# Kernel optimization log

Measured on AMD Instinct MI355X. Metric: run time of the kernel, lower is better.

The kernel has to match this reference:

```python
import jax, jax.numpy as jnp
import numpy as np

N = 100000   # nodes
E = 1600000  # edges
G = 1024     # graphs
V = 51       # attr_dims[0]+1 embedding rows (padding_idx=0)
EMB = 32
H = 2        # heads
D = 64       # hidden_dim (per-head out channels)
DC = H * D   # 128 = dim_conv
NEG_GAT = 0.2   # PyG GATConv default negative_slope
NEG_ACT = 0.05  # module's leaky_relu slope
LN_EPS = 1e-5


def setup_inputs() -> dict:
    key = jax.random.key(0)
    ks = jax.random.split(key, 20)
    def nrm(k, shape, scale=0.1):
        return jax.random.normal(k, shape, dtype=jnp.float32) * scale
    x = jax.random.randint(ks[0], (N, 1), 0, V)
    edge_index = jax.random.randint(ks[1], (2, E), 0, N)
    batch_idx = jnp.sort(jax.random.randint(ks[2], (N,), 0, G))
    return {
        'x': x, 'edge_index': edge_index, 'batch_idx': batch_idx,
        'emb': nrm(ks[3], (V, EMB)).at[0].set(0.0),  # padding_idx=0
        'ln_g': jnp.ones((EMB,), jnp.float32), 'ln_b': jnp.zeros((EMB,), jnp.float32),
        'W1': nrm(ks[4], (EMB, DC)), 'a_src1': nrm(ks[5], (H, D)), 'a_dst1': nrm(ks[6], (H, D)), 'b1': nrm(ks[7], (DC,)),
        'W2': nrm(ks[8], (DC, DC)), 'a_src2': nrm(ks[9], (H, D)), 'a_dst2': nrm(ks[10], (H, D)), 'b2': nrm(ks[11], (DC,)),
        'gw1': nrm(ks[12], (DC, D)), 'gb1': nrm(ks[13], (D,)),
        'gw2': nrm(ks[14], (D, 1)), 'gb2': nrm(ks[15], (1,)),
    }


def _gat_conv(xf, src, dst, W, a_src, a_dst, b):
    # xf: [N, in]; returns [N, H*D]. PyG GATConv, eval mode (attn dropout off).
    xw = (xf @ W).reshape(N, H, D)                           # [N,H,D]
    al_s = jnp.einsum('nhd,hd->nh', xw, a_src)
    al_d = jnp.einsum('nhd,hd->nh', xw, a_dst)
    e = jax.nn.leaky_relu(al_s[src] + al_d[dst], NEG_GAT)    # [E',H]
    m = jax.ops.segment_max(e, dst, num_segments=N)
    ex = jnp.exp(e - m[dst])
    s = jax.ops.segment_sum(ex, dst, num_segments=N)
    alpha = ex / s[dst]                                      # segment softmax over incoming edges
    msg = xw[src] * alpha[:, :, None]                        # [E',H,D]
    out = jax.ops.segment_sum(msg, dst, num_segments=N)      # [N,H,D]
    return out.reshape(N, DC) + b


def reference(x, edge_index, batch_idx, emb, ln_g, ln_b,
              W1, a_src1, a_dst1, b1, W2, a_src2, a_dst2, b2,
              gw1, gb1, gw2, gb2):
    # embedding + LayerNorm (dropout off in eval)
    xe = emb[x[:, 0]]                                        # [N,32]
    mu = jnp.mean(xe, axis=-1, keepdims=True)
    var = jnp.var(xe, axis=-1, keepdims=True)
    xe = (xe - mu) * jax.lax.rsqrt(var + LN_EPS) * ln_g + ln_b
    # add self loops (GATConv add_self_loops=True)
    ar = jnp.arange(N, dtype=edge_index.dtype)
    src = jnp.concatenate([edge_index[0], ar])
    dst = jnp.concatenate([edge_index[1], ar])
    h = jax.nn.leaky_relu(_gat_conv(xe, src, dst, W1, a_src1, a_dst1, b1), NEG_ACT)
    h = _gat_conv(h, src, dst, W2, a_src2, a_dst2, b2)       # [N,128]
    # attentional aggregation over graphs
    gate = jax.nn.leaky_relu(h @ gw1 + gb1, NEG_ACT) @ gw2 + gb2   # [N,1]
    gm = jax.ops.segment_max(gate, batch_idx, num_segments=G)
    ge = jnp.exp(gate - gm[batch_idx])
    gs = jax.ops.segment_sum(ge, batch_idx, num_segments=G)
    w = ge / gs[batch_idx]
    z = jax.ops.segment_sum(w * h, batch_idx, num_segments=G)      # [G,128]
    return h, z
```

## Files before the change

kernel.cpp:

```cpp
#include <hip/hip_runtime.h>
#include <hip/hip_bf16.h>
#include <stdint.h>

typedef unsigned short u16;
typedef unsigned int   u32;
typedef __attribute__((ext_vector_type(8))) short bf16x8;
typedef __attribute__((ext_vector_type(4))) float f32x4;

#define NEG_GAT 0.2f
#define NEG_ACT 0.05f
#define LN_EPS  1e-5f
#define NPARAM  15

__device__ __forceinline__ float bf2f(u32 bits16){
  union { u32 u; float f; } v; v.u = bits16 << 16; return v.f;
}
__device__ __forceinline__ u16 f2bf(float f){
  union { float f; u32 u; } v; v.f = f;
  u32 u = v.u;
  u32 r = (u + 0x7fffu + ((u >> 16) & 1u)) >> 16;
  return (u16)r;
}
__device__ __forceinline__ float lrelu(float x, float s){ return x > 0.f ? x : s * x; }

__device__ __forceinline__ int geti(const int* __restrict__ p, int i, int enc){
  return p[enc ? (2 * i) : i];
}


struct CvtParams {
  const void* src[NPARAM];
  float*      dst[NPARAM];
  int         n[NPARAM];
};

__global__ void k_detect(const u32* __restrict__ ln_g_raw, const int* __restrict__ ei_raw,
                         int* __restrict__ fflag, int* __restrict__ iflag,
                         int* __restrict__ errflag)
{
  if (threadIdx.x == 0){
    *fflag = (ln_g_raw[0] == 0x3F800000u) ? 0 : 1;
    int zeros = 0;
    for (int j = 0; j < 64; j++) if (ei_raw[2 * j + 1] == 0) zeros++;
    *iflag = (zeros >= 60) ? 1 : 0;
    *errflag = 0;
  }
}

__global__ void k_convert(CvtParams P, const int* __restrict__ flag)
{
  const int pi  = blockIdx.y;
  const int idx = blockIdx.x * 256 + threadIdx.x;
  if (idx >= P.n[pi]) return;
  if (*flag == 0) P.dst[pi][idx] = ((const float*)P.src[pi])[idx];
  else            P.dst[pi][idx] = bf2f(((const u16*)P.src[pi])[idx]);
}


__global__ void k_check_sorted(const int* __restrict__ batch, const int* __restrict__ iflag,
                               int n, int* __restrict__ errflag)
{
  int i = blockIdx.x * 256 + threadIdx.x;
  if (i < n - 1){
    if (geti(batch, i, *iflag) > geti(batch, i + 1, *iflag)) atomicOr(errflag, 8);
  }
}

__global__ void k_check_x(const int* __restrict__ x, const int* __restrict__ iflag,
                          int n, int V, int* __restrict__ errflag)
{
  int i = blockIdx.x * 256 + threadIdx.x;
  if (i < n){
    int v = geti(x, i, *iflag);
    if ((unsigned)v >= (unsigned)V) atomicOr(errflag, 16);
  }
}

__global__ void k_check_edges(const int* __restrict__ ei, const int* __restrict__ iflag,
                              int E, int n, int* __restrict__ errflag)
{
  int e = blockIdx.x * 256 + threadIdx.x;
  if (e < E){
    int enc = *iflag;
    int s = geti(ei, e, enc);
    int d = geti(ei, E + e, enc);
    if ((unsigned)s >= (unsigned)n || (unsigned)d >= (unsigned)n) atomicOr(errflag, 32);
  }
}


__global__ void k_hist(const int* __restrict__ ei, const int* __restrict__ iflag,
                       int* __restrict__ counts, int E, int n)
{
  int e = blockIdx.x * 256 + threadIdx.x;
  if (e < E){
    int d = geti(ei, E + e, *iflag);
    d = min(max(d, 0), n - 1);
    atomicAdd(&counts[d], 1);
  }
}

__global__ void k_scanA(const int* __restrict__ counts, int* __restrict__ rowptr,
                        int* __restrict__ bsums, int n)
{
  __shared__ int sd[1024];
  int tid = threadIdx.x;
  int gid = blockIdx.x * 1024 + tid;
  int v = (gid < n) ? counts[gid] : 0;
  sd[tid] = v;
  __syncthreads();
  for (int off = 1; off < 1024; off <<= 1){
    int t = 0;
    if (tid >= off) t = sd[tid - off];
    __syncthreads();
    if (tid >= off) sd[tid] += t;
    __syncthreads();
  }
  if (gid < n) rowptr[gid] = sd[tid] - v;
  if (tid == 1023) bsums[blockIdx.x] = sd[1023];
}

__global__ void k_scanB(const int* __restrict__ bsums, int* __restrict__ boffs, int nb)
{
  __shared__ int sd[128];
  int tid = threadIdx.x;
  int v = (tid < nb) ? bsums[tid] : 0;
  sd[tid] = v;
  __syncthreads();
  for (int off = 1; off < 128; off <<= 1){
    int t = 0;
    if (tid >= off) t = sd[tid - off];
    __syncthreads();
    if (tid >= off) sd[tid] += t;
    __syncthreads();
  }
  if (tid < nb) boffs[tid] = sd[tid] - v;
}

__global__ void k_scanC(int* __restrict__ rowptr, const int* __restrict__ boffs,
                        int* __restrict__ cursor, int n, int Etot)
{
  int gid = blockIdx.x * 1024 + threadIdx.x;
  if (gid < n){
    int v = rowptr[gid] + boffs[blockIdx.x];
    rowptr[gid] = v;
    cursor[gid] = v;
  }
  if (gid == 0) rowptr[n] = Etot;
}

__global__ void k_scatter(const int* __restrict__ ei, const int* __restrict__ iflag,
                          int* __restrict__ cursor, int* __restrict__ csr, int E, int n)
{
  int e = blockIdx.x * 256 + threadIdx.x;
  if (e < E){
    int enc = *iflag;
    int s = geti(ei, e, enc);
    int d = geti(ei, E + e, enc);
    d = min(max(d, 0), n - 1);
    int pos = atomicAdd(&cursor[d], 1);
    csr[pos] = s;
  }
}

__global__ void k_check_rows(const int* __restrict__ rowptr, const int* __restrict__ cursor,
                             int n, int* __restrict__ errflag)
{
  int i = blockIdx.x * 256 + threadIdx.x;
  if (i < n){
    if (cursor[i] != rowptr[i + 1]) atomicOr(errflag, 1);
    if (i == 0 && rowptr[0] != 0)   atomicOr(errflag, 4);
  }
}

__global__ void k_check_csr(const int* __restrict__ csr, int E, int n, int* __restrict__ errflag)
{
  int e = blockIdx.x * 256 + threadIdx.x;
  if (e < E && (unsigned)csr[e] >= (unsigned)n) atomicOr(errflag, 2);
}


#define BSH   9
#define BSZ   512
#define BMSK  511
#define MAXB  2048
#define BINB  8192
#define BTH   512

__global__ void k_bhist(const int* __restrict__ ei, const int* __restrict__ iflag,
                        int* __restrict__ bcnt, int E, int N, int nbuck)
{
  __shared__ int h[MAXB];
  const int t = threadIdx.x;
  for (int i = t; i < nbuck; i += 256) h[i] = 0;
  __syncthreads();
  const int enc = *iflag;
  for (int e = blockIdx.x * 256 + t; e < E; e += gridDim.x * 256){
    int d = geti(ei, E + e, enc);
    d = min(max(d, 0), N - 1);
    atomicAdd(&h[d >> BSH], 1);
  }
  __syncthreads();
  for (int i = t; i < nbuck; i += 256){
    int c = h[i];
    if (c) atomicAdd(&bcnt[i], c);
  }
}

__global__ void k_bscan(const int* __restrict__ bcnt, int* __restrict__ boff,
                        int* __restrict__ gcur, int* __restrict__ rowptr,
                        int nbuck, int N, int E)
{
  __shared__ int sd[MAXB];
  const int lane = threadIdx.x;
  for (int i = lane; i < nbuck; i += 64) sd[i] = bcnt[i];
  __syncthreads();
  const int L = (nbuck + 63) >> 6;
  const int b0 = lane * L;
  int sum = 0;
  for (int j = 0; j < L; j++){ int idx = b0 + j; if (idx < nbuck) sum += sd[idx]; }
  int excl = sum;
  for (int off = 1; off < 64; off <<= 1){
    int x = __shfl_up(excl, off);
    if (lane >= off) excl += x;
  }
  excl -= sum;
  int run = excl;
  for (int j = 0; j < L; j++){
    int idx = b0 + j;
    if (idx < nbuck){ boff[idx] = run; gcur[idx] = run; run += sd[idx]; }
  }
  if (lane == 0){ boff[nbuck] = E; rowptr[N] = E; }
}

__global__ __launch_bounds__(BTH) void k_bbin(
    const int* __restrict__ ei, const int* __restrict__ iflag,
    int* __restrict__ gcur, u32* __restrict__ binned,
    int E, int N, int nbuck)
{
  __shared__ u32 stage[BINB];
  __shared__ u16 sbk[BINB];
  __shared__ int hist[MAXB];
  __shared__ int base[MAXB];
  __shared__ int gpos[MAXB];
  const int t   = threadIdx.x;
  const int e0  = blockIdx.x * BINB;
  const int cnt = min(BINB, E - e0);
  const int enc = *iflag;

  for (int i = t; i < nbuck; i += BTH) hist[i] = 0;
  __syncthreads();

  u32 pv[16]; int bk[16]; int rk[16];
  #pragma unroll
  for (int k = 0; k < 16; k++){
    bk[k] = -1;
    int lo = k * BTH + t;
    if (lo < cnt){
      int e = e0 + lo;
      int s = geti(ei, e, enc);
      int d = geti(ei, E + e, enc);
      s = min(max(s, 0), N - 1);
      d = min(max(d, 0), N - 1);
      int b = d >> BSH;
      pv[k] = ((u32)s << BSH) | (u32)(d & BMSK);
      bk[k] = b;
      rk[k] = atomicAdd(&hist[b], 1);
    }
  }
  __syncthreads();

  if (t < 64){
    const int L = (nbuck + 63) >> 6;
    const int b0 = t * L;
    int sum = 0;
    for (int j = 0; j < L; j++){ int idx = b0 + j; if (idx < nbuck) sum += hist[idx]; }
    int excl = sum;
    for (int off = 1; off < 64; off <<= 1){
      int x = __shfl_up(excl, off);
      if (t >= off) excl += x;
    }
    excl -= sum;
    int run = excl;
    for (int j = 0; j < L; j++){
      int idx = b0 + j;
      if (idx < nbuck){ base[idx] = run; run += hist[idx]; }
    }
  }
  __syncthreads();

  for (int i = t; i < nbuck; i += BTH){
    int c = hist[i];
    gpos[i] = c ? atomicAdd(&gcur[i], c) : 0;
  }
  __syncthreads();

  #pragma unroll
  for (int k = 0; k < 16; k++){
    if (bk[k] >= 0){
      int slot = base[bk[k]] + rk[k];
      stage[slot] = pv[k];
      sbk[slot]   = (u16)bk[k];
    }
  }
  __syncthreads();

  for (int j = t; j < cnt; j += BTH){
    int b = sbk[j];
    binned[gpos[b] + (j - base[b])] = stage[j];
  }
}

__global__ __launch_bounds__(256) void k_bcsr(
    const u32* __restrict__ binned, const int* __restrict__ boff,
    int* __restrict__ rowptr, int* __restrict__ csr, int N, int nbuck)
{
  __shared__ int cnt[BSZ];
  __shared__ int rp[BSZ];
  __shared__ int cur[BSZ];
  const int b = blockIdx.x;
  const int t = threadIdx.x;
  const int lo = boff[b], hi = boff[b + 1];

  for (int i = t; i < BSZ; i += 256){ cnt[i] = 0; cur[i] = 0; }
  __syncthreads();

  for (int j = lo + t; j < hi; j += 256)
    atomicAdd(&cnt[binned[j] & BMSK], 1);
  __syncthreads();

  if (t < 64){
    const int b0 = t * 8;
    int sum = 0;
    #pragma unroll
    for (int j = 0; j < 8; j++) sum += cnt[b0 + j];
    int excl = sum;
    for (int off = 1; off < 64; off <<= 1){
      int x = __shfl_up(excl, off);
      if (t >= off) excl += x;
    }
    excl -= sum;
    int run = excl;
    #pragma unroll
    for (int j = 0; j < 8; j++){ rp[b0 + j] = run; run += cnt[b0 + j]; }
  }
  __syncthreads();

  const int node0 = b << BSH;
  for (int i = t; i < BSZ; i += 256){
    int node = node0 + i;
    if (node < N) rowptr[node] = lo + rp[i];
  }

  for (int j = lo + t; j < hi; j += 256){
    u32 pvv = binned[j];
    int dl  = pvv & BMSK;
    int pos = lo + rp[dl] + atomicAdd(&cur[dl], 1);
    csr[pos] = (int)(pvv >> BSH);
  }
}


__global__ void k_stamp_if(const int* __restrict__ errflag, float* __restrict__ out, int nel)
{
  int f = *errflag;
  if (f == 0) return;
  float s = 500.0f + 100.0f * (float)f;
  int i = blockIdx.x * 256 + threadIdx.x;
  if (i < nel) out[i] = s;
}

__global__ void k_stamp(float* __restrict__ out, int nel, float val)
{
  int i = blockIdx.x * 256 + threadIdx.x;
  if (i < nel) out[i] = val;
}


__global__ void k_prep(const float* __restrict__ emb,
                       const float* __restrict__ ln_g, const float* __restrict__ ln_b,
                       const float* __restrict__ W1, const float* __restrict__ a_src,
                       const float* __restrict__ a_dst,
                       u16* __restrict__ xwv, float* __restrict__ alsv, float* __restrict__ aldv)
{
  __shared__ float se[32];
  __shared__ float stats[2];
  __shared__ float sxw[128];
  const int v = blockIdx.x, t = threadIdx.x;
  if (t < 32) se[t] = emb[v * 32 + t];
  __syncthreads();
  if (t == 0){
    float s1 = 0.f, s2 = 0.f;
    for (int k = 0; k < 32; k++){ s1 += se[k]; s2 += se[k] * se[k]; }
    float mu = s1 * (1.f / 32.f);
    float var = s2 * (1.f / 32.f) - mu * mu;
    stats[0] = mu; stats[1] = rsqrtf(var + LN_EPS);
  }
  __syncthreads();
  const float mu = stats[0], rs = stats[1];
  float o = 0.f;
  for (int k = 0; k < 32; k++){
    float xe = (se[k] - mu) * rs * ln_g[k] + ln_b[k];
    o += xe * W1[k * 128 + t];
  }
  sxw[t] = o;
  xwv[v * 128 + t] = f2bf(o);
  __syncthreads();
  if (t < 2){
    float ps = 0.f, pd = 0.f;
    for (int d = 0; d < 64; d++){
      float vv = sxw[t * 64 + d];
      ps += vv * a_src[t * 64 + d];
      pd += vv * a_dst[t * 64 + d];
    }
    alsv[2 * v + t] = ps;
    aldv[2 * v + t] = pd;
  }
}

__global__ void k_lookup(const int* __restrict__ x, const int* __restrict__ iflag,
                         const u16* __restrict__ xwv, const float* __restrict__ alsv,
                         const float* __restrict__ aldv, int N, int V,
                         u16* __restrict__ xw, float* __restrict__ al_s, float* __restrict__ al_d)
{
  const int enc = *iflag;
  const int tid = threadIdx.x;
  const int c = tid & 15;
  for (int base = blockIdx.x * 16; base < N; base += gridDim.x * 16){
    int i = base + (tid >> 4);
    if (i < N){
      int v = geti(x, i, enc);
      v = min(max(v, 0), V - 1);
      uint4 row = *(const uint4*)(xwv + v * 128 + c * 8);
      *(uint4*)(xw + (size_t)i * 128 + c * 8) = row;
      if (c == 0){ float2 a = *(const float2*)(alsv + 2 * v); *(float2*)(al_s + 2 * i) = a; }
      if (c == 1){ float2 a = *(const float2*)(aldv + 2 * v); *(float2*)(al_d + 2 * i) = a; }
    }
  }
}


__global__ __launch_bounds__(64, 8) void k_gatw(
    const int* __restrict__ rowptr, const int* __restrict__ csr,
    const float* __restrict__ al_s, const float* __restrict__ al_d,
    const u16* __restrict__ xw, const float* __restrict__ bias,
    int apply_act, float* __restrict__ out)
{
  const int i    = blockIdx.x;
  const int lane = threadIdx.x;
  const int sub  = lane >> 4;
  const int c16  = lane & 15;
  const int r0 = rowptr[i], deg = rowptr[i + 1] - r0, total = deg + 1;
  const float ad0 = al_d[2 * i], ad1 = al_d[2 * i + 1];

  float m0 = -3.0e38f, m1 = -3.0e38f;
  for (int k = lane; k < total; k += 64){
    int s = (k < deg) ? csr[r0 + k] : i;
    float a0 = lrelu(al_s[2 * s]     + ad0, NEG_GAT);
    float a1 = lrelu(al_s[2 * s + 1] + ad1, NEG_GAT);
    m0 = fmaxf(m0, a0); m1 = fmaxf(m1, a1);
  }
  #pragma unroll
  for (int off = 32; off; off >>= 1){
    m0 = fmaxf(m0, __shfl_xor(m0, off));
    m1 = fmaxf(m1, __shfl_xor(m1, off));
  }

  float sum0 = 0.f, sum1 = 0.f;
  float acc[8];
  #pragma unroll
  for (int r = 0; r < 8; r++) acc[r] = 0.f;

  for (int base = 0; base < total; base += 64){
    int k = base + lane;
    int s = i; float ex0 = 0.f, ex1 = 0.f;
    if (k < total){
      s = (k < deg) ? csr[r0 + k] : i;
      ex0 = __expf(lrelu(al_s[2 * s]     + ad0, NEG_GAT) - m0);
      ex1 = __expf(lrelu(al_s[2 * s + 1] + ad1, NEG_GAT) - m1);
    }
    sum0 += ex0; sum1 += ex1;

    int cnt  = min(64, total - base);
    int qmax = (cnt + 3) & ~3;
    for (int q = 0; q < qmax; q += 4){
      int   j  = q + sub;
      int   sj = __shfl(s, j);
      float e0 = __shfl(ex0, j);
      float e1 = __shfl(ex1, j);
      float ej = (c16 < 8) ? e0 : e1;
      uint4 w = *(const uint4*)(xw + (size_t)sj * 128 + c16 * 8);
      acc[0] += ej * bf2f(w.x & 0xffffu); acc[1] += ej * bf2f(w.x >> 16);
      acc[2] += ej * bf2f(w.y & 0xffffu); acc[3] += ej * bf2f(w.y >> 16);
      acc[4] += ej * bf2f(w.z & 0xffffu); acc[5] += ej * bf2f(w.z >> 16);
      acc[6] += ej * bf2f(w.w & 0xffffu); acc[7] += ej * bf2f(w.w >> 16);
    }
  }
  #pragma unroll
  for (int off = 32; off; off >>= 1){
    sum0 += __shfl_xor(sum0, off);
    sum1 += __shfl_xor(sum1, off);
  }
  #pragma unroll
  for (int r = 0; r < 8; r++){
    acc[r] += __shfl_xor(acc[r], 16);
    acc[r] += __shfl_xor(acc[r], 32);
  }

  if (sub == 0){
    float inv = 1.f / ((c16 < 8) ? sum0 : sum1);
    const float4* bp = (const float4*)(bias + c16 * 8);
    float4 b0 = bp[0], b1 = bp[1];
    float4 o0, o1;
    o0.x = acc[0] * inv + b0.x; o0.y = acc[1] * inv + b0.y;
    o0.z = acc[2] * inv + b0.z; o0.w = acc[3] * inv + b0.w;
    o1.x = acc[4] * inv + b1.x; o1.y = acc[5] * inv + b1.y;
    o1.z = acc[6] * inv + b1.z; o1.w = acc[7] * inv + b1.w;
    if (apply_act){
      o0.x = lrelu(o0.x, NEG_ACT); o0.y = lrelu(o0.y, NEG_ACT);
      o0.z = lrelu(o0.z, NEG_ACT); o0.w = lrelu(o0.w, NEG_ACT);
      o1.x = lrelu(o1.x, NEG_ACT); o1.y = lrelu(o1.y, NEG_ACT);
      o1.z = lrelu(o1.z, NEG_ACT); o1.w = lrelu(o1.w, NEG_ACT);
    }
    float* op = out + (size_t)i * 128 + c16 * 8;
    *(float4*)op       = o0;
    *(float4*)(op + 4) = o1;
  }
}


__global__ void k_packW(const float* __restrict__ W, int ncols, int ntiles,
                        u16* __restrict__ pb)
{
  const int ktile = blockIdx.x / ntiles;
  const int ntile = blockIdx.x % ntiles;
  const int lane  = threadIdx.x;
  const int n  = ntile * 16 + (lane & 15);
  const int k0 = ktile * 32 + (lane >> 4) * 8;
  u16* dst = pb + ((size_t)blockIdx.x * 64 + lane) * 8;
  #pragma unroll
  for (int j = 0; j < 8; j++)
    dst[j] = f2bf(W[(k0 + j) * ncols + n]);
}


__global__ __launch_bounds__(256, 2) void k_node2m(
    const float* __restrict__ h1, const u16* __restrict__ pb2,
    const float* __restrict__ a_src, const float* __restrict__ a_dst,
    int N, u16* __restrict__ xw, float* __restrict__ al_s, float* __restrict__ al_d)
{
  const int wave = threadIdx.x >> 6;
  const int lane = threadIdx.x & 63;
  const int rowbase = blockIdx.x * 64 + wave * 16;
  const int m    = lane & 15;
  const int quad = lane >> 4;

  int arow = rowbase + m; if (arow >= N) arow = N - 1;
  const float* aptr = h1 + (size_t)arow * 128 + quad * 8;

  f32x4 acc[8];
  #pragma unroll
  for (int nt = 0; nt < 8; nt++) acc[nt] = (f32x4){0.f, 0.f, 0.f, 0.f};

  #pragma unroll
  for (int kt = 0; kt < 4; kt++){
    float4 a0 = *(const float4*)(aptr + kt * 32);
    float4 a1 = *(const float4*)(aptr + kt * 32 + 4);
    bf16x8 af;
    af[0] = (short)f2bf(a0.x); af[1] = (short)f2bf(a0.y);
    af[2] = (short)f2bf(a0.z); af[3] = (short)f2bf(a0.w);
    af[4] = (short)f2bf(a1.x); af[5] = (short)f2bf(a1.y);
    af[6] = (short)f2bf(a1.z); af[7] = (short)f2bf(a1.w);
    const u16* bbase = pb2 + (((size_t)kt * 8) * 64 + lane) * 8;
    #pragma unroll
    for (int nt = 0; nt < 8; nt++){
      bf16x8 bf = *(const bf16x8*)(bbase + (size_t)nt * 64 * 8);
      acc[nt] = __builtin_amdgcn_mfma_f32_16x16x32_bf16(af, bf, acc[nt], 0, 0, 0);
    }
  }

  float asv[8], adv[8];
  #pragma unroll
  for (int nt = 0; nt < 8; nt++){
    asv[nt] = a_src[nt * 16 + m];
    adv[nt] = a_dst[nt * 16 + m];
  }
  #pragma unroll
  for (int r = 0; r < 4; r++){
    int row = rowbase + quad * 4 + r;
    bool ok = row < N;
    float s0 = 0.f, s1 = 0.f, d0 = 0.f, d1 = 0.f;
    #pragma unroll
    for (int nt = 0; nt < 8; nt++){
      float v = acc[nt][r];
      if (ok) xw[(size_t)row * 128 + nt * 16 + m] = f2bf(v);
      if (nt < 4){ s0 += v * asv[nt]; d0 += v * adv[nt]; }
      else       { s1 += v * asv[nt]; d1 += v * adv[nt]; }
    }
    #pragma unroll
    for (int off = 1; off < 16; off <<= 1){
      s0 += __shfl_xor(s0, off); s1 += __shfl_xor(s1, off);
      d0 += __shfl_xor(d0, off); d1 += __shfl_xor(d1, off);
    }
    if (ok && m == 0){
      al_s[2 * row] = s0; al_s[2 * row + 1] = s1;
      al_d[2 * row] = d0; al_d[2 * row + 1] = d1;
    }
  }
}


__global__ __launch_bounds__(256, 2) void k_gatem(
    const float* __restrict__ h, const u16* __restrict__ pbg,
    const float* __restrict__ gb1, const float* __restrict__ gw2,
    const float* __restrict__ gb2, int N, float* __restrict__ gate)
{
  const int wave = threadIdx.x >> 6;
  const int lane = threadIdx.x & 63;
  const int rowbase = blockIdx.x * 64 + wave * 16;
  const int m    = lane & 15;
  const int quad = lane >> 4;

  int arow = rowbase + m; if (arow >= N) arow = N - 1;
  const float* aptr = h + (size_t)arow * 128 + quad * 8;

  f32x4 acc[4];
  #pragma unroll
  for (int nt = 0; nt < 4; nt++) acc[nt] = (f32x4){0.f, 0.f, 0.f, 0.f};

  #pragma unroll
  for (int kt = 0; kt < 4; kt++){
    float4 a0 = *(const float4*)(aptr + kt * 32);
    float4 a1 = *(const float4*)(aptr + kt * 32 + 4);
    bf16x8 af;
    af[0] = (short)f2bf(a0.x); af[1] = (short)f2bf(a0.y);
    af[2] = (short)f2bf(a0.z); af[3] = (short)f2bf(a0.w);
    af[4] = (short)f2bf(a1.x); af[5] = (short)f2bf(a1.y);
    af[6] = (short)f2bf(a1.z); af[7] = (short)f2bf(a1.w);
    const u16* bbase = pbg + (((size_t)kt * 4) * 64 + lane) * 8;
    #pragma unroll
    for (int nt = 0; nt < 4; nt++){
      bf16x8 bf = *(const bf16x8*)(bbase + (size_t)nt * 64 * 8);
      acc[nt] = __builtin_amdgcn_mfma_f32_16x16x32_bf16(af, bf, acc[nt], 0, 0, 0);
    }
  }

  float gbv[4], g2v[4];
  #pragma unroll
  for (int nt = 0; nt < 4; nt++){
    gbv[nt] = gb1[nt * 16 + m];
    g2v[nt] = gw2[nt * 16 + m];
  }
  const float g2b = gb2[0];
  #pragma unroll
  for (int r = 0; r < 4; r++){
    int row = rowbase + quad * 4 + r;
    float q = 0.f;
    #pragma unroll
    for (int nt = 0; nt < 4; nt++)
      q += lrelu(acc[nt][r] + gbv[nt], NEG_ACT) * g2v[nt];
    #pragma unroll
    for (int off = 1; off < 16; off <<= 1) q += __shfl_xor(q, off);
    if (row < N && m == 0) gate[row] = q + g2b;
  }
}


__global__ void k_graphsw(const int* __restrict__ batch, const int* __restrict__ iflag,
                          const float* __restrict__ gate,
                          const float* __restrict__ h, float* __restrict__ zout, int N)
{
  __shared__ int   range[2];
  __shared__ float red[4];
  const int g = blockIdx.x, t = threadIdx.x;
  const int wave = t >> 6;
  if (t == 0){
    const int enc = *iflag;
    int lo = 0, hi = N;
    while (lo < hi){ int mid = (lo + hi) >> 1; if (geti(batch, mid, enc) < g) lo = mid + 1; else hi = mid; }
    range[0] = lo;
    hi = N;
    while (lo < hi){ int mid = (lo + hi) >> 1; if (geti(batch, mid, enc) < g + 1) lo = mid + 1; else hi = mid; }
    range[1] = lo;
  }
  __syncthreads();
  const int st = range[0], en = range[1];

  float m = -3.0e38f;
  for (int k = st + t; k < en; k += 128) m = fmaxf(m, gate[k]);
  #pragma unroll
  for (int off = 32; off; off >>= 1) m = fmaxf(m, __shfl_xor(m, off));
  if ((t & 63) == 0) red[wave] = m;
  __syncthreads();
  m = fmaxf(red[0], red[1]);

  float s = 0.f;
  for (int k = st + t; k < en; k += 128) s += __expf(gate[k] - m);
  #pragma unroll
  for (int off = 32; off; off >>= 1) s += __shfl_xor(s, off);
  if ((t & 63) == 0) red[2 + wave] = s;
  __syncthreads();
  s = red[2] + red[3];

  float z = 0.f;
  const float inv = 1.f / s;
  for (int k = st; k < en; k++){
    float wk = __expf(gate[k] - m) * inv;
    z += wk * h[(size_t)k * 128 + t];
  }
  zout[(size_t)g * 128 + t] = z;
}


extern "C" void kernel_launch(void* const* d_in, const int* in_sizes, int n_in,
                              void* d_out, int out_size, void* d_ws, size_t ws_size,
                              hipStream_t stream)
{
  const int* x      = (const int*)d_in[0];
  const int* ei     = (const int*)d_in[1];
  const int* batch  = (const int*)d_in[2];

  const int N = in_sizes[0];
  const int E = in_sizes[1] / 2;
  const int V = in_sizes[3] / 32;
  const int G = out_size / 128 - N;

  char* p = (char*)d_ws;
  auto alloc = [&](size_t bytes) -> char* {
    char* r = p; p += (bytes + 255) & ~(size_t)255; return r;
  };
  int*   multi  = (int*)  alloc((size_t)N * 4);
  int*   rowptr = (int*)  alloc((size_t)(N + 1) * 4);
  int*   csr    = (int*)  alloc((size_t)E * 4);
  int*   bsums  = (int*)  alloc(4096);
  int*   boffs  = (int*)  alloc(4096);
  int*   flags  = (int*)  alloc(256);
  int*   fflag  = flags;
  int*   iflag  = flags + 1;
  int*   errflg = flags + 2;
  float* al_s   = (float*)alloc((size_t)N * 2 * 4);
  float* al_d   = (float*)alloc((size_t)N * 2 * 4);
  u16*   xw     = (u16*)  alloc((size_t)N * 128 * 2);
  u16*   xwv    = (u16*)  alloc((size_t)V * 128 * 2);
  float* alsv   = (float*)alloc((size_t)V * 2 * 4);
  float* aldv   = (float*)alloc((size_t)V * 2 * 4);
  u16*   pb2    = (u16*)  alloc((size_t)128 * 128 * 2);
  u16*   pbg    = (u16*)  alloc((size_t)128 * 64 * 2);

  const int nbuck = (N + BSZ - 1) >> BSH;
  int*   bcnt   = (int*)  alloc((size_t)(MAXB) * 4);
  int*   boff   = (int*)  alloc((size_t)(MAXB + 1) * 4);
  int*   gcur   = (int*)  alloc((size_t)(MAXB) * 4);
  u32*   binned = (u32*)  alloc((size_t)E * 4);

  CvtParams cp;
  float* fpar[NPARAM];
  int maxn = 0;
  for (int pi = 0; pi < NPARAM; pi++){
    int n = in_sizes[3 + pi];
    fpar[pi] = (float*)alloc((size_t)n * 4);
    cp.src[pi] = d_in[3 + pi];
    cp.dst[pi] = fpar[pi];
    cp.n[pi]   = n;
    if (n > maxn) maxn = n;
  }
  const size_t needed = (size_t)(p - (char*)d_ws);

  const float* emb    = fpar[0];
  const float* ln_g   = fpar[1];
  const float* ln_b   = fpar[2];
  const float* W1     = fpar[3];
  const float* a_src1 = fpar[4];
  const float* a_dst1 = fpar[5];
  const float* b1     = fpar[6];
  const float* W2     = fpar[7];
  const float* a_src2 = fpar[8];
  const float* a_dst2 = fpar[9];
  const float* b2     = fpar[10];
  const float* gw1    = fpar[11];
  const float* gb1    = fpar[12];
  const float* gw2    = fpar[13];
  const float* gb2    = fpar[14];
  (void)n_in;

  int ob = (out_size + 255) / 256;
  if (ws_size < needed){
    k_stamp<<<ob, 256, 0, stream>>>((float*)d_out, out_size, 9999.0f);
    return;
  }

  int*   counts = multi;
  int*   cursor = multi;
  float* gate   = (float*)multi;
  float* hbuf   = (float*)d_out;
  float* zbuf   = (float*)d_out + (size_t)N * 128;

  k_detect<<<1, 64, 0, stream>>>((const u32*)d_in[4], ei, fflag, iflag, errflg);
  dim3 cgrid((maxn + 255) / 256, NPARAM);
  k_convert<<<cgrid, 256, 0, stream>>>(cp, fflag);

  int eb = (E + 255) / 256;
  int nb = (N + 1023) / 1024;
  int nb256 = (N + 255) / 256;

  k_check_sorted<<<nb256, 256, 0, stream>>>(batch, iflag, N, errflg);
  k_check_x<<<nb256, 256, 0, stream>>>(x, iflag, N, V, errflg);
  k_check_edges<<<eb, 256, 0, stream>>>(ei, iflag, E, N, errflg);

  if (nbuck <= MAXB){
    hipMemsetAsync(bcnt, 0, (size_t)nbuck * 4, stream);
    k_bhist<<<256, 256, 0, stream>>>(ei, iflag, bcnt, E, N, nbuck);
    k_bscan<<<1, 64, 0, stream>>>(bcnt, boff, gcur, rowptr, nbuck, N, E);
    k_bbin<<<(E + BINB - 1) / BINB, BTH, 0, stream>>>(ei, iflag, gcur, binned, E, N, nbuck);
    k_bcsr<<<nbuck, 256, 0, stream>>>(binned, boff, rowptr, csr, N, nbuck);
  } else {
    hipMemsetAsync(counts, 0, (size_t)N * 4, stream);
    hipMemsetAsync(csr, 0xFF, (size_t)E * 4, stream);
    k_hist<<<eb, 256, 0, stream>>>(ei, iflag, counts, E, N);
    k_scanA<<<nb, 1024, 0, stream>>>(counts, rowptr, bsums, N);
    k_scanB<<<1, 128, 0, stream>>>(bsums, boffs, nb);
    k_scanC<<<nb, 1024, 0, stream>>>(rowptr, boffs, cursor, N, E);
    k_scatter<<<eb, 256, 0, stream>>>(ei, iflag, cursor, csr, E, N);
    k_check_rows<<<nb256, 256, 0, stream>>>(rowptr, cursor, N, errflg);
    k_check_csr<<<eb, 256, 0, stream>>>(csr, E, N, errflg);
  }

  k_packW<<<32, 64, 0, stream>>>(W2, 128, 8, pb2);
  k_packW<<<16, 64, 0, stream>>>(gw1, 64, 4, pbg);

  k_prep<<<V, 128, 0, stream>>>(emb, ln_g, ln_b, W1, a_src1, a_dst1, xwv, alsv, aldv);
  k_lookup<<<1024, 256, 0, stream>>>(x, iflag, xwv, alsv, aldv, N, V, xw, al_s, al_d);

  k_gatw<<<N, 64, 0, stream>>>(rowptr, csr, al_s, al_d, xw, b1, 1, hbuf);

  const int gblk = (N + 63) / 64;
  k_node2m<<<gblk, 256, 0, stream>>>(hbuf, pb2, a_src2, a_dst2, N, xw, al_s, al_d);

  k_gatw<<<N, 64, 0, stream>>>(rowptr, csr, al_s, al_d, xw, b2, 0, hbuf);

  k_gatem<<<gblk, 256, 0, stream>>>(hbuf, pbg, gb1, gw2, gb2, N, gate);
  k_graphsw<<<G, 128, 0, stream>>>(batch, iflag, gate, hbuf, zbuf, N);

  k_stamp_if<<<ob, 256, 0, stream>>>(errflg, (float*)d_out, out_size);
}
```

Measured before the change: 421.4 us.

## Fuse embedding lookup into first GAT layer and single-pass softmax for small degrees

```diff
diff --git a/kernel.cpp b/kernel.cpp
--- a/kernel.cpp
+++ b/kernel.cpp
@@ -21,7 +21,7 @@
   u32 r = (u + 0x7fffu + ((u >> 16) & 1u)) >> 16;
   return (u16)r;
 }
-__device__ __forceinline__ float lrelu(float x, float s){ return x > 0.f ? x : s * x; }
+__device__ __forceinline__ float lrelu(float x, float s){ return fmaxf(x, s * x); }
 
 __device__ __forceinline__ int geti(const int* __restrict__ p, int i, int enc){
   return p[enc ? (2 * i) : i];
@@ -418,29 +418,131 @@
   }
 }
 
-__global__ void k_lookup(const int* __restrict__ x, const int* __restrict__ iflag,
-                         const u16* __restrict__ xwv, const float* __restrict__ alsv,
-                         const float* __restrict__ aldv, int N, int V,
-                         u16* __restrict__ xw, float* __restrict__ al_s, float* __restrict__ al_d)
-{
-  const int enc = *iflag;
-  const int tid = threadIdx.x;
-  const int c = tid & 15;
-  for (int base = blockIdx.x * 16; base < N; base += gridDim.x * 16){
-    int i = base + (tid >> 4);
-    if (i < N){
-      int v = geti(x, i, enc);
-      v = min(max(v, 0), V - 1);
-      uint4 row = *(const uint4*)(xwv + v * 128 + c * 8);
-      *(uint4*)(xw + (size_t)i * 128 + c * 8) = row;
-      if (c == 0){ float2 a = *(const float2*)(alsv + 2 * v); *(float2*)(al_s + 2 * i) = a; }
-      if (c == 1){ float2 a = *(const float2*)(aldv + 2 * v); *(float2*)(al_d + 2 * i) = a; }
-    }
-  }
-}
-
-
-__global__ __launch_bounds__(64, 8) void k_gatw(
+
+__global__ __launch_bounds__(64, 8) void k_gatw1(
+    const int* __restrict__ rowptr, const int* __restrict__ csr,
+    const int* __restrict__ x, const int* __restrict__ iflag,
+    const float* __restrict__ alsv, const float* __restrict__ aldv,
+    const u16* __restrict__ xwv, const float* __restrict__ bias,
+    int V, float* __restrict__ out)
+{
+  const int i    = blockIdx.x;
+  const int lane = threadIdx.x;
+  const int sub  = lane >> 4;
+  const int c16  = lane & 15;
+  const int enc  = *iflag;
+  const int r0 = rowptr[i], deg = rowptr[i + 1] - r0, total = deg + 1;
+  int vi = geti(x, i, enc); vi = min(max(vi, 0), V - 1);
+  const float ad0 = aldv[2 * vi], ad1 = aldv[2 * vi + 1];
+
+  float sum0 = 0.f, sum1 = 0.f;
+  float acc[8];
+  #pragma unroll
+  for (int r = 0; r < 8; r++) acc[r] = 0.f;
+
+  if (total <= 64){
+    int vs = vi;
+    float a0 = -3.0e38f, a1 = -3.0e38f;
+    if (lane < total){
+      int s = (lane < deg) ? csr[r0 + lane] : i;
+      int v = geti(x, s, enc);
+      vs = min(max(v, 0), V - 1);
+      float2 as = *(const float2*)(alsv + 2 * vs);
+      a0 = lrelu(as.x + ad0, NEG_GAT);
+      a1 = lrelu(as.y + ad1, NEG_GAT);
+    }
+    float m0 = a0, m1 = a1;
+    #pragma unroll
+    for (int off = 32; off; off >>= 1){
+      m0 = fmaxf(m0, __shfl_xor(m0, off));
+      m1 = fmaxf(m1, __shfl_xor(m1, off));
+    }
+    float ex0 = 0.f, ex1 = 0.f;
+    if (lane < total){ ex0 = __expf(a0 - m0); ex1 = __expf(a1 - m1); }
+    sum0 = ex0; sum1 = ex1;
+    int qmax = (total + 3) & ~3;
+    for (int q = 0; q < qmax; q += 4){
+      int   j  = q + sub;
+      int   vj = __shfl(vs, j);
+      float e0 = __shfl(ex0, j);
+      float e1 = __shfl(ex1, j);
+      float ej = (c16 < 8) ? e0 : e1;
+      uint4 w = *(const uint4*)(xwv + (size_t)vj * 128 + c16 * 8);
+      acc[0] += ej * bf2f(w.x & 0xffffu); acc[1] += ej * bf2f(w.x >> 16);
+      acc[2] += ej * bf2f(w.y & 0xffffu); acc[3] += ej * bf2f(w.y >> 16);
+      acc[4] += ej * bf2f(w.z & 0xffffu); acc[5] += ej * bf2f(w.z >> 16);
+      acc[6] += ej * bf2f(w.w & 0xffffu); acc[7] += ej * bf2f(w.w >> 16);
+    }
+  } else {
+    float m0 = -3.0e38f, m1 = -3.0e38f;
+    for (int k = lane; k < total; k += 64){
+      int s = (k < deg) ? csr[r0 + k] : i;
+      int v = geti(x, s, enc); v = min(max(v, 0), V - 1);
+      float2 as = *(const float2*)(alsv + 2 * v);
+      m0 = fmaxf(m0, lrelu(as.x + ad0, NEG_GAT));
+      m1 = fmaxf(m1, lrelu(as.y + ad1, NEG_GAT));
+    }
+    #pragma unroll
+    for (int off = 32; off; off >>= 1){
+      m0 = fmaxf(m0, __shfl_xor(m0, off));
+      m1 = fmaxf(m1, __shfl_xor(m1, off));
+    }
+    for (int base = 0; base < total; base += 64){
+      int k = base + lane;
+      int vs = vi; float ex0 = 0.f, ex1 = 0.f;
+      if (k < total){
+        int s = (k < deg) ? csr[r0 + k] : i;
+        int v = geti(x, s, enc); vs = min(max(v, 0), V - 1);
+        float2 as = *(const float2*)(alsv + 2 * vs);
+        ex0 = __expf(lrelu(as.x + ad0, NEG_GAT) - m0);
+        ex1 = __expf(lrelu(as.y + ad1, NEG_GAT) - m1);
+      }
+      sum0 += ex0; sum1 += ex1;
+      int cnt = min(64, total - base);
+      int qmax = (cnt + 3) & ~3;
+      for (int q = 0; q < qmax; q += 4){
+        int   j  = q + sub;
+        int   vj = __shfl(vs, j);
+        float e0 = __shfl(ex0, j);
+        float e1 = __shfl(ex1, j);
+        float ej = (c16 < 8) ? e0 : e1;
+        uint4 w = *(const uint4*)(xwv + (size_t)vj * 128 + c16 * 8);
+        acc[0] += ej * bf2f(w.x & 0xffffu); acc[1] += ej * bf2f(w.x >> 16);
+        acc[2] += ej * bf2f(w.y & 0xffffu); acc[3] += ej * bf2f(w.y >> 16);
+        acc[4] += ej * bf2f(w.z & 0xffffu); acc[5] += ej * bf2f(w.z >> 16);
+        acc[6] += ej * bf2f(w.w & 0xffffu); acc[7] += ej * bf2f(w.w >> 16);
+      }
+    }
+  }
+
+  #pragma unroll
+  for (int off = 32; off; off >>= 1){
+    sum0 += __shfl_xor(sum0, off);
+    sum1 += __shfl_xor(sum1, off);
+  }
+  #pragma unroll
+  for (int r = 0; r < 8; r++){
+    acc[r] += __shfl_xor(acc[r], 16);
+    acc[r] += __shfl_xor(acc[r], 32);
+  }
+
+  if (sub == 0){
+    float inv = 1.f / ((c16 < 8) ? sum0 : sum1);
+    const float4* bp = (const float4*)(bias + c16 * 8);
+    float4 b0 = bp[0], b1 = bp[1];
+    float4 o0, o1;
+    o0.x = lrelu(acc[0] * inv + b0.x, NEG_ACT); o0.y = lrelu(acc[1] * inv + b0.y, NEG_ACT);
+    o0.z = lrelu(acc[2] * inv + b0.z, NEG_ACT); o0.w = lrelu(acc[3] * inv + b0.w, NEG_ACT);
+    o1.x = lrelu(acc[4] * inv + b1.x, NEG_ACT); o1.y = lrelu(acc[5] * inv + b1.y, NEG_ACT);
+    o1.z = lrelu(acc[6] * inv + b1.z, NEG_ACT); o1.w = lrelu(acc[7] * inv + b1.w, NEG_ACT);
+    float* op = out + (size_t)i * 128 + c16 * 8;
+    *(float4*)op       = o0;
+    *(float4*)(op + 4) = o1;
+  }
+}
+
+
+__global__ __launch_bounds__(64, 8) void k_gatw2(
     const int* __restrict__ rowptr, const int* __restrict__ csr,
     const float* __restrict__ al_s, const float* __restrict__ al_d,
     const u16* __restrict__ xw, const float* __restrict__ bias,
@@ -451,38 +553,32 @@
   const int sub  = lane >> 4;
   const int c16  = lane & 15;
   const int r0 = rowptr[i], deg = rowptr[i + 1] - r0, total = deg + 1;
-  const float ad0 = al_d[2 * i], ad1 = al_d[2 * i + 1];
-
-  float m0 = -3.0e38f, m1 = -3.0e38f;
-  for (int k = lane; k < total; k += 64){
-    int s = (k < deg) ? csr[r0 + k] : i;
-    float a0 = lrelu(al_s[2 * s]     + ad0, NEG_GAT);
-    float a1 = lrelu(al_s[2 * s + 1] + ad1, NEG_GAT);
-    m0 = fmaxf(m0, a0); m1 = fmaxf(m1, a1);
-  }
-  #pragma unroll
-  for (int off = 32; off; off >>= 1){
-    m0 = fmaxf(m0, __shfl_xor(m0, off));
-    m1 = fmaxf(m1, __shfl_xor(m1, off));
-  }
+  const float2 ad = *(const float2*)(al_d + 2 * i);
 
   float sum0 = 0.f, sum1 = 0.f;
   float acc[8];
   #pragma unroll
   for (int r = 0; r < 8; r++) acc[r] = 0.f;
 
-  for (int base = 0; base < total; base += 64){
-    int k = base + lane;
-    int s = i; float ex0 = 0.f, ex1 = 0.f;
-    if (k < total){
-      s = (k < deg) ? csr[r0 + k] : i;
-      ex0 = __expf(lrelu(al_s[2 * s]     + ad0, NEG_GAT) - m0);
-      ex1 = __expf(lrelu(al_s[2 * s + 1] + ad1, NEG_GAT) - m1);
-    }
-    sum0 += ex0; sum1 += ex1;
-
-    int cnt  = min(64, total - base);
-    int qmax = (cnt + 3) & ~3;
+  if (total <= 64){
+    int s = i;
+    float a0 = -3.0e38f, a1 = -3.0e38f;
+    if (lane < total){
+      s = (lane < deg) ? csr[r0 + lane] : i;
+      float2 as = *(const float2*)(al_s + 2 * s);
+      a0 = lrelu(as.x + ad.x, NEG_GAT);
+      a1 = lrelu(as.y + ad.y, NEG_GAT);
+    }
+    float m0 = a0, m1 = a1;
+    #pragma unroll
+    for (int off = 32; off; off >>= 1){
+      m0 = fmaxf(m0, __shfl_xor(m0, off));
+      m1 = fmaxf(m1, __shfl_xor(m1, off));
+    }
+    float ex0 = 0.f, ex1 = 0.f;
+    if (lane < total){ ex0 = __expf(a0 - m0); ex1 = __expf(a1 - m1); }
+    sum0 = ex0; sum1 = ex1;
+    int qmax = (total + 3) & ~3;
     for (int q = 0; q < qmax; q += 4){
       int   j  = q + sub;
       int   sj = __shfl(s, j);
@@ -495,7 +591,46 @@
       acc[4] += ej * bf2f(w.z & 0xffffu); acc[5] += ej * bf2f(w.z >> 16);
       acc[6] += ej * bf2f(w.w & 0xffffu); acc[7] += ej * bf2f(w.w >> 16);
     }
-  }
+  } else {
+    float m0 = -3.0e38f, m1 = -3.0e38f;
+    for (int k = lane; k < total; k += 64){
+      int s = (k < deg) ? csr[r0 + k] : i;
+      float2 as = *(const float2*)(al_s + 2 * s);
+      m0 = fmaxf(m0, lrelu(as.x + ad.x, NEG_GAT));
+      m1 = fmaxf(m1, lrelu(as.y + ad.y, NEG_GAT));
+    }
+    #pragma unroll
+    for (int off = 32; off; off >>= 1){
+      m0 = fmaxf(m0, __shfl_xor(m0, off));
+      m1 = fmaxf(m1, __shfl_xor(m1, off));
+    }
+    for (int base = 0; base < total; base += 64){
+      int k = base + lane;
+      int s = i; float ex0 = 0.f, ex1 = 0.f;
+      if (k < total){
+        s = (k < deg) ? csr[r0 + k] : i;
+        float2 as = *(const float2*)(al_s + 2 * s);
+        ex0 = __expf(lrelu(as.x + ad.x, NEG_GAT) - m0);
+        ex1 = __expf(lrelu(as.y + ad.y, NEG_GAT) - m1);
+      }
+      sum0 += ex0; sum1 += ex1;
+      int cnt = min(64, total - base);
+      int qmax = (cnt + 3) & ~3;
+      for (int q = 0; q < qmax; q += 4){
+        int   j  = q + sub;
+        int   sj = __shfl(s, j);
+        float e0 = __shfl(ex0, j);
+        float e1 = __shfl(ex1, j);
+        float ej = (c16 < 8) ? e0 : e1;
+        uint4 w = *(const uint4*)(xw + (size_t)sj * 128 + c16 * 8);
+        acc[0] += ej * bf2f(w.x & 0xffffu); acc[1] += ej * bf2f(w.x >> 16);
+        acc[2] += ej * bf2f(w.y & 0xffffu); acc[3] += ej * bf2f(w.y >> 16);
+        acc[4] += ej * bf2f(w.z & 0xffffu); acc[5] += ej * bf2f(w.z >> 16);
+        acc[6] += ej * bf2f(w.w & 0xffffu); acc[7] += ej * bf2f(w.w >> 16);
+      }
+    }
+  }
+
   #pragma unroll
   for (int off = 32; off; off >>= 1){
     sum0 += __shfl_xor(sum0, off);
@@ -829,14 +964,12 @@
   k_packW<<<16, 64, 0, stream>>>(gw1, 64, 4, pbg);
 
   k_prep<<<V, 128, 0, stream>>>(emb, ln_g, ln_b, W1, a_src1, a_dst1, xwv, alsv, aldv);
-  k_lookup<<<1024, 256, 0, stream>>>(x, iflag, xwv, alsv, aldv, N, V, xw, al_s, al_d);
-
-  k_gatw<<<N, 64, 0, stream>>>(rowptr, csr, al_s, al_d, xw, b1, 1, hbuf);
+  k_gatw1<<<N, 64, 0, stream>>>(rowptr, csr, x, iflag, alsv, aldv, xwv, b1, V, hbuf);
 
   const int gblk = (N + 63) / 64;
   k_node2m<<<gblk, 256, 0, stream>>>(hbuf, pb2, a_src2, a_dst2, N, xw, al_s, al_d);
 
-  k_gatw<<<N, 64, 0, stream>>>(rowptr, csr, al_s, al_d, xw, b2, 0, hbuf);
+  k_gatw2<<<N, 64, 0, stream>>>(rowptr, csr, al_s, al_d, xw, b2, 0, hbuf);
 
   k_gatem<<<gblk, 256, 0, stream>>>(hbuf, pbg, gb1, gw2, gb2, N, gate);
   k_graphsw<<<G, 128, 0, stream>>>(batch, iflag, gate, hbuf, zbuf, N);
```

After: 398.4 us. 1.06x faster.
